# Optimization experiments

Hardware: AMD Instinct MI355X
Metric: run time of the kernel (lower is better)

Reference implementation:

```python
import jax, jax.numpy as jnp
import numpy as np

BSZ, DIM, H, W = 4, 128, 64, 64
D_MODEL = 128
D = 128   # d_expand == d_inner
N = 16    # d_state
R = 8     # dt_rank = ceil(128/16)
K = 4     # scan directions
L = H * W


def _ln_last(x, g, b, eps):
    m = x.mean(-1, keepdims=True)
    v = x.var(-1, keepdims=True)
    return (x - m) * jax.lax.rsqrt(v + eps) * g + b


def _ln_channel(x, g, b, eps):
    # LayerNorm2d: normalize over channel axis of NCHW
    m = x.mean(1, keepdims=True)
    v = x.var(1, keepdims=True)
    return (x - m) * jax.lax.rsqrt(v + eps) * g[None, :, None, None] + b[None, :, None, None]


def _cross_scan(x):
    # x: (B, D, H, W) -> (B, K, D, L); dirs: row-major, col-major, and their reverses
    b, d = x.shape[0], x.shape[1]
    x0 = x.reshape(b, d, L)
    x1 = x.transpose(0, 1, 3, 2).reshape(b, d, L)
    return jnp.stack([x0, x1, x0[..., ::-1], x1[..., ::-1]], axis=1)


def _cross_merge(ys):
    # ys: (B, K, D, L) -> (B, D, L)
    b, _, d, _ = ys.shape
    ys = ys[:, 0:2] + ys[:, 2:4, :, ::-1]
    y1 = ys[:, 1].reshape(b, d, W, H).transpose(0, 1, 3, 2).reshape(b, d, L)
    return ys[:, 0] + y1


def _selective_scan(u, dt, A, Bs, Cs, Dsk):
    # u, dt: (B,K,D,L); A: (K,D,N); Bs, Cs: (B,K,N,L); Dsk: (K,D)
    uT = u.transpose(3, 0, 1, 2)    # (L,B,K,D)
    dtT = dt.transpose(3, 0, 1, 2)
    BT = Bs.transpose(3, 0, 1, 2)   # (L,B,K,N)
    CT = Cs.transpose(3, 0, 1, 2)
    h0 = jnp.zeros((u.shape[0], K, u.shape[2], N), u.dtype)

    def step(h, inp):
        ut, dtt, bt, ct = inp
        dA = jnp.exp(dtt[..., None] * A)                      # (B,K,D,N)
        h = dA * h + (dtt * ut)[..., None] * bt[:, :, None, :]
        y = jnp.sum(h * ct[:, :, None, :], axis=-1)           # (B,K,D)
        return h, y

    _, ysT = jax.lax.scan(step, h0, (uT, dtT, BT, CT))
    ys = ysT.transpose(1, 2, 3, 0)                            # (B,K,D,L)
    return ys + u * Dsk[None, :, :, None]


def _forward(x, in_proj_w, conv_w, conv_b, sa_w, sa_b, x_proj_weight,
             dt_projs_weight, dt_projs_bias, A_logs, Ds,
             out_norm_g, out_norm_b, norm1_g, norm1_b, out_proj_w):
    # in_proj (1x1 conv, no bias) then chunk into x, z
    xz = jnp.einsum('bchw,oc->bohw', x, in_proj_w)
    xi, z = jnp.split(xz, 2, axis=1)
    z1 = jax.nn.gelu(z, approximate=False)
    # depthwise 3x3 conv + bias
    xi = jax.lax.conv_general_dilated(xi, conv_w, (1, 1), 'SAME',
                                      feature_group_count=D,
                                      dimension_numbers=('NCHW', 'OIHW', 'NCHW'))
    xi = xi + conv_b[None, :, None, None]
    xi = jax.nn.gelu(xi, approximate=False)
    # SpatialAttention (CBAM-style): mean+max over channels -> 7x7 conv -> sigmoid gate
    pooled = jnp.concatenate([xi.mean(1, keepdims=True), xi.max(1, keepdims=True)], axis=1)
    attn = jax.lax.conv_general_dilated(pooled, sa_w, (1, 1), 'SAME',
                                        dimension_numbers=('NCHW', 'OIHW', 'NCHW'))
    xi = xi * jax.nn.sigmoid(attn + sa_b[None, :, None, None])
    # cross selective scan
    xs = _cross_scan(xi)                                              # (B,K,D,L)
    x_dbl = jnp.einsum('bkdl,kcd->bkcl', xs, x_proj_weight)           # (B,K,R+2N,L)
    dts, Bs, Cs = x_dbl[:, :, :R], x_dbl[:, :, R:R + N], x_dbl[:, :, R + N:]
    dts = jnp.einsum('bkrl,kdr->bkdl', dts, dt_projs_weight)
    dt = jax.nn.softplus(dts + dt_projs_bias[None, :, :, None])
    A = -jnp.exp(A_logs).reshape(K, D, N)
    ys = _selective_scan(xs, dt, A, Bs, Cs, Ds.reshape(K, D))         # (B,K,D,L)
    y = _cross_merge(ys)                                              # (B,D,L)
    y = y.reshape(-1, D, H, W).transpose(0, 2, 3, 1)                  # (B,H,W,D)
    y = _ln_last(y, out_norm_g, out_norm_b, 1e-5)
    y = y.transpose(0, 3, 1, 2)                                       # (B,D,H,W)
    # z gate, LayerNorm2d, out_proj (1x1 conv)
    y = y * z1
    y = _ln_channel(y, norm1_g, norm1_b, 1e-6)
    return jnp.einsum('bchw,oc->bohw', y, out_proj_w)


def setup_inputs() -> dict:
    key = jax.random.key(0)
    ks = jax.random.split(key, 8)
    s = 0.02
    return {
        'x': jax.random.normal(ks[0], (BSZ, DIM, H, W), jnp.float32),
        'in_proj_w': jax.random.normal(ks[1], (2 * D, DIM), jnp.float32) * s,
        'conv_w': jax.random.normal(ks[2], (D, 1, 3, 3), jnp.float32) * s,
        'conv_b': jnp.zeros((D,), jnp.float32),
        'sa_w': jax.random.normal(ks[3], (1, 2, 7, 7), jnp.float32) * s,
        'sa_b': jnp.zeros((1,), jnp.float32),
        'x_proj_weight': jax.random.normal(ks[4], (K, R + 2 * N, D), jnp.float32) * s,
        'dt_projs_weight': jax.random.normal(ks[5], (K, D, R), jnp.float32) * s,
        'dt_projs_bias': jax.random.normal(ks[6], (K, D), jnp.float32) * s,
        'A_logs': jnp.log(jnp.tile(jnp.arange(1, N + 1, dtype=jnp.float32)[None, :], (K * D, 1))),
        'Ds': jnp.ones((K * D,), jnp.float32),
        'out_norm_g': jnp.ones((D,), jnp.float32),
        'out_norm_b': jnp.zeros((D,), jnp.float32),
        'norm1_g': jnp.ones((D,), jnp.float32),
        'norm1_b': jnp.zeros((D,), jnp.float32),
        'out_proj_w': jax.random.normal(ks[7], (D_MODEL, D), jnp.float32) * s,
    }


def reference(x, in_proj_w, conv_w, conv_b, sa_w, sa_b, x_proj_weight,
              dt_projs_weight, dt_projs_bias, A_logs, Ds,
              out_norm_g, out_norm_b, norm1_g, norm1_b, out_proj_w):
    return _forward(x, in_proj_w, conv_w, conv_b, sa_w, sa_b, x_proj_weight,
                    dt_projs_weight, dt_projs_bias, A_logs, Ds,
                    out_norm_g, out_norm_b, norm1_g, norm1_b, out_proj_w)
```

## Files before the change

### kernel.cpp

```cpp
#include <hip/hip_runtime.h>
#include <math.h>

#define BB   4
#define DD   128
#define LL   4096
#define SEG  128

union F4 { float4 v; float f[4]; };

__device__ __forceinline__ float gelu_f(float x){
  return 0.5f * x * (1.f + erff(x * 0.70710678118654752f));
}
__device__ __forceinline__ float softplus_fast(float x){
  return (x > 20.f) ? x : __logf(1.f + __expf(x));
}

__global__ __launch_bounds__(256) void k_inproj(const float* __restrict__ x,
    const float* __restrict__ W, float* __restrict__ xi, float* __restrict__ z1){
  __shared__ __align__(16) float Xs[128*32];
  int b = blockIdx.z; int half = blockIdx.y; int p0 = blockIdx.x*32;
  int t = threadIdx.x;
  int po = t & 31, row8 = t >> 5;
  for (int j=0;j<16;j++){
    int c = row8 + 8*j;
    Xs[c*32 + po] = x[((size_t)(b*128 + c))*LL + p0 + po];
  }
  __syncthreads();
  int pg = t & 7, og = t >> 3;
  int obase = og*4 + half*128;
  const float4* w0r = (const float4*)&W[(size_t)(obase+0)*128];
  const float4* w1r = (const float4*)&W[(size_t)(obase+1)*128];
  const float4* w2r = (const float4*)&W[(size_t)(obase+2)*128];
  const float4* w3r = (const float4*)&W[(size_t)(obase+3)*128];
  float acc[4][4];
  #pragma unroll
  for (int i=0;i<4;i++){ acc[i][0]=0;acc[i][1]=0;acc[i][2]=0;acc[i][3]=0; }
  for (int c4=0;c4<32;c4++){
    F4 xv[4];
    #pragma unroll
    for (int r=0;r<4;r++) xv[r].v = *(const float4*)&Xs[(c4*4+r)*32 + pg*4];
    F4 wv[4];
    wv[0].v = w0r[c4]; wv[1].v = w1r[c4]; wv[2].v = w2r[c4]; wv[3].v = w3r[c4];
    #pragma unroll
    for (int i=0;i<4;i++)
      #pragma unroll
      for (int q=0;q<4;q++)
        acc[i][q] = fmaf(wv[i].f[3], xv[3].f[q],
                    fmaf(wv[i].f[2], xv[2].f[q],
                    fmaf(wv[i].f[1], xv[1].f[q],
                    fmaf(wv[i].f[0], xv[0].f[q], acc[i][q]))));
  }
  if (half == 0){
    #pragma unroll
    for (int i=0;i<4;i++){
      F4 st; st.f[0]=acc[i][0]; st.f[1]=acc[i][1]; st.f[2]=acc[i][2]; st.f[3]=acc[i][3];
      *(float4*)&xi[((size_t)(b*128+obase+i))*LL + p0 + pg*4] = st.v;
    }
  } else {
    #pragma unroll
    for (int i=0;i<4;i++){
      F4 st; st.f[0]=gelu_f(acc[i][0]); st.f[1]=gelu_f(acc[i][1]);
      st.f[2]=gelu_f(acc[i][2]); st.f[3]=gelu_f(acc[i][3]);
      *(float4*)&z1[((size_t)(b*128+obase-128+i))*LL + p0 + pg*4] = st.v;
    }
  }
}

__global__ __launch_bounds__(256) void k_conv(const float* __restrict__ xi,
    const float* __restrict__ cw, const float* __restrict__ cb, float* __restrict__ xc){
  int idx = blockIdx.x*256 + threadIdx.x;
  int p = idx & 4095; int c = (idx>>12) & 127; int b = idx>>19;
  int y = p>>6, x = p&63;
  const float* src = xi + ((size_t)(b*128+c))*LL;
  float w[9];
  #pragma unroll
  for (int i=0;i<9;i++) w[i] = cw[c*9+i];
  float a = cb[c];
  #pragma unroll
  for (int dy=-1;dy<=1;dy++){
    int yy = y+dy; if (yy<0 || yy>63) continue;
    #pragma unroll
    for (int dx=-1;dx<=1;dx++){
      int xx = x+dx; if (xx<0 || xx>63) continue;
      a = fmaf(w[(dy+1)*3+dx+1], src[yy*64+xx], a);
    }
  }
  xc[((size_t)(b*128+c))*LL + p] = gelu_f(a);
}

__global__ __launch_bounds__(256) void k_pool(const float* __restrict__ xc,
    float* __restrict__ pooled){
  __shared__ float rs[4][64], rm[4][64];
  int b = blockIdx.y; int po = threadIdx.x & 63; int cg = threadIdx.x >> 6;
  int p = blockIdx.x*64 + po;
  const float* src = xc + ((size_t)b*128)*LL + p;
  float s = 0.f, mx = -3.4e38f;
  for (int ci=0;ci<32;ci++){
    float v = src[(size_t)(cg*32+ci)*LL];
    s += v; mx = fmaxf(mx, v);
  }
  rs[cg][po] = s; rm[cg][po] = mx;
  __syncthreads();
  if (cg == 0){
    float ss = rs[0][po]+rs[1][po]+rs[2][po]+rs[3][po];
    float mm = fmaxf(fmaxf(rm[0][po],rm[1][po]),fmaxf(rm[2][po],rm[3][po]));
    pooled[((size_t)(b*2+0))*LL + p] = ss*(1.f/128.f);
    pooled[((size_t)(b*2+1))*LL + p] = mm;
  }
}

__global__ __launch_bounds__(256) void k_attn(const float* __restrict__ pooled,
    const float* __restrict__ saw, const float* __restrict__ sab, float* __restrict__ sig){
  __shared__ float ps[2][10][70];
  int b = blockIdx.y; int p0 = blockIdx.x*256;
  int y0 = p0>>6;
  int t = threadIdx.x;
  for (int e=t; e<1400; e+=256){
    int ic = e/700; int rem = e - ic*700; int r = rem/70; int cc = rem - r*70;
    int gy = y0-3+r, gx = cc-3;
    float v = 0.f;
    if (gy>=0&&gy<64&&gx>=0&&gx<64) v = pooled[((size_t)(b*2+ic))*LL + gy*64+gx];
    ps[ic][r][cc] = v;
  }
  __syncthreads();
  int ry = t>>6, xx = t&63;
  float acc = sab[0];
  #pragma unroll
  for (int ic=0;ic<2;ic++)
    for (int ky=0;ky<7;ky++)
      #pragma unroll
      for (int kx=0;kx<7;kx++)
        acc += saw[ic*49+ky*7+kx] * ps[ic][ry+ky][xx+kx];
  sig[(size_t)b*LL + p0 + t] = 1.f/(1.f+__expf(-acc));
}

__global__ __launch_bounds__(256) void k_gate(const float* __restrict__ xc,
    const float* __restrict__ sig, float* __restrict__ u, float* __restrict__ uT){
  __shared__ float tl[64*65];
  int d = blockIdx.x, b = blockIdx.y;
  const float* src = xc + ((size_t)(b*128+d))*LL;
  const float* sg  = sig + (size_t)b*LL;
  float* du = u  + ((size_t)(b*128+d))*LL;
  float* dT = uT + ((size_t)(b*128+d))*LL;
  int t = threadIdx.x;
  #pragma unroll
  for (int j=0;j<16;j++){
    int idx = t + j*256;
    int r = idx>>6, c = idx&63;
    float v = src[idx]*sg[idx];
    du[idx] = v;
    tl[c*65+r] = v;
  }
  __syncthreads();
  #pragma unroll
  for (int j=0;j<16;j++){
    int idx = t + j*256;
    int r = idx>>6, c = idx&63;
    dT[idx] = tl[r*65+c];
  }
}

__global__ __launch_bounds__(256) void k_gate4(const float* __restrict__ u,
    const float* __restrict__ uT, float* __restrict__ u4){
  __shared__ float T[64*130];
  int tile = blockIdx.x;
  int ori  = blockIdx.y;
  int b    = blockIdx.z;
  const float* src = (ori ? uT : u) + ((size_t)b*128)*LL + tile*64;
  int t = threadIdx.x;
  int po = t&63, dg = t>>6;
  for (int di=0; di<32; di++){
    int d = dg*32+di;
    T[po*130 + d] = src[(size_t)d*LL + po];
  }
  __syncthreads();
  float* dst = u4 + ((size_t)((b*2+ori)*1024) + tile*16)*512;
  #pragma unroll
  for (int j=0;j<8;j++){
    int L = j*1024 + t*4;
    int d = t & 127;
    int pxb = (L >> 9)*4;
    F4 st;
    #pragma unroll
    for (int s=0;s<4;s++) st.f[s] = T[(pxb+s)*130 + d];
    *(float4*)&dst[L] = st.v;
  }
}

__global__ __launch_bounds__(256) void k_xdbl(const float* __restrict__ u,
    const float* __restrict__ uT, const float* __restrict__ xpw,
    float* __restrict__ C8_l, float* __restrict__ Bs_l, float* __restrict__ Cs_l){
  __shared__ __align__(16) float Ws[40*128];
  __shared__ __align__(16) float Xs[64*128];
  __shared__ __align__(16) float Xd[40*128];
  int px0 = blockIdx.x*128;
  int k = blockIdx.y; int b = blockIdx.z; int bk = b*4+k;
  int t = threadIdx.x;
  const float* ub = (k&1) ? uT : u;
  {
    const float4* src = (const float4*)(xpw + (size_t)k*40*128);
    float4* dst = (float4*)Ws;
    #pragma unroll
    for (int j=0;j<5;j++) dst[t + j*256] = src[t + j*256];
  }
  int pg = t&31, rg = t>>5;
  float acc[5][4];
  #pragma unroll
  for (int i=0;i<5;i++){ acc[i][0]=0;acc[i][1]=0;acc[i][2]=0;acc[i][3]=0; }
  for (int h=0;h<2;h++){
    __syncthreads();
    {
      int p4 = t&31, ch = t>>5;
      #pragma unroll
      for (int j=0;j<8;j++){
        int c = ch + j*8;
        F4 v; v.v = *(const float4*)&ub[((size_t)(b*128 + h*64 + c))*LL + px0 + p4*4];
        *(float4*)&Xs[c*128 + p4*4] = v.v;
      }
    }
    __syncthreads();
    const float* wbase = Ws + rg*5*128 + h*64;
    for (int c4=0;c4<16;c4++){
      F4 xv[4];
      #pragma unroll
      for (int r=0;r<4;r++) xv[r].v = *(const float4*)&Xs[(c4*4+r)*128 + pg*4];
      F4 wv[5];
      #pragma unroll
      for (int i=0;i<5;i++) wv[i].v = *(const float4*)(wbase + i*128 + c4*4);
      #pragma unroll
      for (int i=0;i<5;i++)
        #pragma unroll
        for (int q=0;q<4;q++)
          acc[i][q] = fmaf(wv[i].f[3], xv[3].f[q],
                      fmaf(wv[i].f[2], xv[2].f[q],
                      fmaf(wv[i].f[1], xv[1].f[q],
                      fmaf(wv[i].f[0], xv[0].f[q], acc[i][q]))));
    }
  }
  #pragma unroll
  for (int i=0;i<5;i++){
    F4 st; st.f[0]=acc[i][0]; st.f[1]=acc[i][1]; st.f[2]=acc[i][2]; st.f[3]=acc[i][3];
    *(float4*)&Xd[(rg*5+i)*128 + pg*4] = st.v;
  }
  __syncthreads();
  #pragma unroll
  for (int j=0;j<5;j++){
    int idx = t + j*256;
    int row = idx>>5, pq = idx&31;
    F4 v; v.v = *(const float4*)&Xd[row*128 + pq*4];
    float* dst;
    if (row < 8)       dst = C8_l + ((size_t)(bk*8 + row))*LL;
    else if (row < 24) dst = Bs_l + ((size_t)(bk*16 + row-8))*LL;
    else               dst = Cs_l + ((size_t)(bk*16 + row-24))*LL;
    int pp = px0 + pq*4;
    if (k < 2){
      *(float4*)&dst[pp] = v.v;
    } else {
      F4 st; st.f[0]=v.f[3]; st.f[1]=v.f[2]; st.f[2]=v.f[1]; st.f[3]=v.f[0];
      *(float4*)&dst[LL-4-pp] = st.v;
    }
  }
}

__global__ __launch_bounds__(256) void k_dt(const float* __restrict__ C8_l,
    const float* __restrict__ dtw, const float* __restrict__ dtb,
    float* __restrict__ dt4){
  __shared__ __align__(16) F4 c8s[8*16];
  __shared__ float wt[128*9];
  __shared__ float db[128];
  int chunk = blockIdx.x;
  int bk = blockIdx.y; int k = bk&3;
  int t = threadIdx.x;
  int px0 = chunk*64;
  if (t < 128){
    c8s[t].v = *(const float4*)&C8_l[((size_t)(bk*8 + (t>>4)))*LL + px0 + (t&15)*4];
    db[t] = dtb[k*128 + t];
  }
  {
    const float* src = dtw + (size_t)k*128*8;
    #pragma unroll
    for (int j=0;j<4;j++){
      int e = t + j*256;
      wt[(e>>3)*9 + (e&7)] = src[e];
    }
  }
  __syncthreads();
  float* outb = dt4 + ((size_t)(bk*1024 + chunk*16))*512;
  #pragma unroll
  for (int j=0;j<8;j++){
    int idx = j*256 + t;
    int i4l = idx>>7, d = idx&127;
    float dw[8];
    #pragma unroll
    for (int r=0;r<8;r++) dw[r] = wt[d*9+r];
    float bias = db[d];
    float a0=bias, a1=bias, a2=bias, a3=bias;
    #pragma unroll
    for (int r=0;r<8;r++){
      F4 c = c8s[r*16 + i4l];
      a0 = fmaf(dw[r], c.f[0], a0);
      a1 = fmaf(dw[r], c.f[1], a1);
      a2 = fmaf(dw[r], c.f[2], a2);
      a3 = fmaf(dw[r], c.f[3], a3);
    }
    F4 st;
    st.f[0]=softplus_fast(a0); st.f[1]=softplus_fast(a1);
    st.f[2]=softplus_fast(a2); st.f[3]=softplus_fast(a3);
    *(float4*)&outb[(size_t)i4l*512 + d*4] = st.v;
  }
}

__global__ __launch_bounds__(256) void k_scan1(const float* __restrict__ dt4,
    const float* __restrict__ u4,
    const float* __restrict__ Bs_l, const float* __restrict__ A_logs,
    float* __restrict__ Ebuf, float* __restrict__ sdtbuf){
  int t = threadIdx.x;
  int lane = t & 63; int dh = (t>>6)&1; int segl = t>>7;
  int seg = blockIdx.x*2 + segl; int bk = blockIdx.y;
  int b = bk>>2, k = bk&3;
  int d = dh*64 + lane;
  float A2[16];
  {
    const float4* al = (const float4*)&A_logs[((size_t)(k*128+d))*16];
    #pragma unroll
    for (int q=0;q<4;q++){
      F4 v; v.v = al[q];
      #pragma unroll
      for (int e=0;e<4;e++) A2[q*4+e] = -__expf(v.f[e]);
    }
  }
  float h[16];
  #pragma unroll
  for (int n=0;n<16;n++) h[n]=0.f;
  float sumdt = 0.f;
  bool rev = (k >= 2);
  const float* dt4p = dt4 + ((size_t)(bk*1024 + seg*8)*128 + d)*4;
  const float* u4b  = u4 + ((size_t)((b*2+(k&1))*1024))*512 + d*4;
  const float* Bn = Bs_l + ((size_t)bk*16)*LL + seg*32;
  for (int i4=0;i4<8;i4++){
    F4 dtv; dtv.v = *(const float4*)(dt4p + i4*512);
    F4 uv;
    if (!rev) uv.v = *(const float4*)(u4b + (size_t)(seg*8 + i4)*512);
    else { F4 t0; t0.v = *(const float4*)(u4b + (size_t)(1023 - seg*8 - i4)*512);
           uv.f[0]=t0.f[3]; uv.f[1]=t0.f[2]; uv.f[2]=t0.f[1]; uv.f[3]=t0.f[0]; }
    F4 Bq[16];
    #pragma unroll
    for (int n=0;n<16;n++) Bq[n].v = *(const float4*)(Bn + (size_t)n*LL + i4*4);
    #pragma unroll
    for (int s=0;s<4;s++){
      float dt = dtv.f[s], uu = uv.f[s];
      float au = dt*uu;
      #pragma unroll
      for (int n=0;n<16;n++) h[n] = __expf(dt*A2[n])*h[n] + au*Bq[n].f[s];
      sumdt += dt;
    }
  }
  size_t eoff = ((size_t)(bk*128 + d))*SEG + seg;
  float* ep = Ebuf + eoff*16;
  #pragma unroll
  for (int q=0;q<4;q++){
    F4 st; st.f[0]=h[q*4+0]; st.f[1]=h[q*4+1]; st.f[2]=h[q*4+2]; st.f[3]=h[q*4+3];
    *(float4*)(ep + q*4) = st.v;
  }
  sdtbuf[eoff] = sumdt;
}

__global__ __launch_bounds__(128) void k_scan2(const float* __restrict__ Ebuf,
    const float* __restrict__ sdtbuf, const float* __restrict__ A_logs,
    float* __restrict__ hin){
  __shared__ float A0s[16], E0s[16];
  int d = blockIdx.x;
  int bk = blockIdx.y;
  int k = bk&3;
  int t = threadIdx.x; int lane = t & 63; int w = t >> 6;
  size_t base = ((size_t)(bk*128+d))*SEG;
  float A2[16];
  {
    const float4* al = (const float4*)&A_logs[((size_t)(k*128+d))*16];
    #pragma unroll
    for (int q=0;q<4;q++){
      F4 v; v.v = al[q];
      #pragma unroll
      for (int e=0;e<4;e++) A2[q*4+e] = -__expf(v.f[e]);
    }
  }
  float sdt = sdtbuf[base + t];
  float a[16], e[16];
  {
    const float* ep = Ebuf + (base+t)*16;
    #pragma unroll
    for (int q=0;q<4;q++){
      F4 v; v.v = *(const float4*)(ep + q*4);
      #pragma unroll
      for (int ee=0;ee<4;ee++) e[q*4+ee]=v.f[ee];
    }
  }
  #pragma unroll
  for (int n=0;n<16;n++) a[n] = __expf(sdt*A2[n]);
  #pragma unroll
  for (int off=1; off<64; off<<=1){
    #pragma unroll
    for (int n=0;n<16;n++){
      float pa = __shfl_up(a[n], off, 64);
      float pe = __shfl_up(e[n], off, 64);
      if (lane >= off){ e[n] = fmaf(a[n], pe, e[n]); a[n] *= pa; }
    }
  }
  if (t == 63){
    #pragma unroll
    for (int n=0;n<16;n++){ A0s[n] = a[n]; E0s[n] = e[n]; }
  }
  __syncthreads();
  float eex[16], aex[16];
  #pragma unroll
  for (int n=0;n<16;n++){
    float pa = __shfl_up(a[n], 1, 64);
    float pe = __shfl_up(e[n], 1, 64);
    aex[n] = lane ? pa : 1.f;
    eex[n] = lane ? pe : 0.f;
  }
  if (w == 1){
    #pragma unroll
    for (int n=0;n<16;n++) eex[n] = fmaf(aex[n], E0s[n], eex[n]);
  }
  float* hp = hin + (base+t)*16;
  #pragma unroll
  for (int q=0;q<4;q++){
    F4 st;
    #pragma unroll
    for (int ee=0;ee<4;ee++) st.f[ee] = eex[q*4+ee];
    *(float4*)(hp + q*4) = st.v;
  }
}

__global__ __launch_bounds__(256) void k_scan3(const float* __restrict__ dt4,
    const float* __restrict__ u4,
    const float* __restrict__ Bs_l, const float* __restrict__ Cs_l,
    const float* __restrict__ A_logs, const float* __restrict__ Ds,
    const float* __restrict__ hin, float* __restrict__ ys4){
  int t = threadIdx.x;
  int lane = t & 63; int dh = (t>>6)&1; int segl = t>>7;
  int seg = blockIdx.x*2 + segl; int bk = blockIdx.y;
  int b = bk>>2, k = bk&3;
  int d = dh*64 + lane;
  float A2[16];
  {
    const float4* al = (const float4*)&A_logs[((size_t)(k*128+d))*16];
    #pragma unroll
    for (int q=0;q<4;q++){
      F4 v; v.v = al[q];
      #pragma unroll
      for (int e=0;e<4;e++) A2[q*4+e] = -__expf(v.f[e]);
    }
  }
  float h[16];
  {
    const float* hp = hin + (((size_t)(bk*128+d))*SEG + seg)*16;
    #pragma unroll
    for (int q=0;q<4;q++){
      F4 v; v.v = *(const float4*)(hp + q*4);
      #pragma unroll
      for (int e=0;e<4;e++) h[q*4+e]=v.f[e];
    }
  }
  float Dd = Ds[k*128+d];
  bool rev = (k >= 2);
  const float* dt4p = dt4 + ((size_t)(bk*1024 + seg*8)*128 + d)*4;
  const float* u4b  = u4 + ((size_t)((b*2+(k&1))*1024))*512 + d*4;
  const float* Bn = Bs_l + ((size_t)bk*16)*LL + seg*32;
  const float* Cn = Cs_l + ((size_t)bk*16)*LL + seg*32;
  float* yo = ys4 + ((size_t)(bk*1024 + seg*8))*512 + d*4;
  for (int i4=0;i4<8;i4++){
    F4 dtv; dtv.v = *(const float4*)(dt4p + i4*512);
    F4 uv;
    if (!rev) uv.v = *(const float4*)(u4b + (size_t)(seg*8 + i4)*512);
    else { F4 t0; t0.v = *(const float4*)(u4b + (size_t)(1023 - seg*8 - i4)*512);
           uv.f[0]=t0.f[3]; uv.f[1]=t0.f[2]; uv.f[2]=t0.f[1]; uv.f[3]=t0.f[0]; }
    F4 Bq[16], Cq[16];
    #pragma unroll
    for (int n=0;n<16;n++){
      Bq[n].v = *(const float4*)(Bn + (size_t)n*LL + i4*4);
      Cq[n].v = *(const float4*)(Cn + (size_t)n*LL + i4*4);
    }
    F4 yv;
    #pragma unroll
    for (int s=0;s<4;s++){
      float dt = dtv.f[s], uu = uv.f[s];
      float au = dt*uu;
      float y = uu*Dd;
      #pragma unroll
      for (int n=0;n<16;n++){
        h[n] = __expf(dt*A2[n])*h[n] + au*Bq[n].f[s];
        y = fmaf(h[n], Cq[n].f[s], y);
      }
      yv.f[s] = y;
    }
    *(float4*)(yo + (size_t)i4*512) = yv.v;
  }
}

__global__ __launch_bounds__(256) void k_tr13(const float* __restrict__ ys4,
    float* __restrict__ y13){
  __shared__ float T[16*516];
  int xg = blockIdx.x & 15, yb = blockIdx.x >> 4, b = blockIdx.y;
  const float* y1 = ys4 + ((size_t)((b*4+1)*1024))*512;
  const float* y3 = ys4 + ((size_t)((b*4+3)*1024))*512;
  int t = threadIdx.x;
  int d = t & 127;
  #pragma unroll
  for (int rr=0; rr<8; rr++){
    int ri = rr*2 + (t>>7);
    int xi = ri>>2, r = ri&3;
    int i4q = (4*xg+xi)*16 + yb*4 + r;
    F4 v1; v1.v = *(const float4*)(y1 + (size_t)i4q*512 + d*4);
    F4 v3; v3.v = *(const float4*)(y3 + (size_t)(1023-i4q)*512 + d*4);
    #pragma unroll
    for (int s=0;s<4;s++)
      T[(4*r+s)*516 + d*4 + xi] = v1.f[s] + v3.f[3-s];
  }
  __syncthreads();
  float* dst = y13 + ((size_t)b*1024)*512;
  #pragma unroll
  for (int rr=0; rr<8; rr++){
    int j = rr*2 + (t>>7);
    F4 o;
    #pragma unroll
    for (int s=0;s<4;s++) o.f[s] = T[j*516 + d*4 + s];
    int i4p = (yb*16 + j)*16 + xg;
    *(float4*)(dst + (size_t)i4p*512 + d*4) = o.v;
  }
}

__global__ __launch_bounds__(256) void k_final(const float* __restrict__ ys4,
    const float* __restrict__ y13,
    const float* __restrict__ z1, const float* __restrict__ ong, const float* __restrict__ onb,
    const float* __restrict__ n1g, const float* __restrict__ n1b,
    const float* __restrict__ W2, float* __restrict__ out){
  __shared__ __align__(16) float yt[128*36];
  __shared__ float red[8][32], redq[8][32], mv[4][32];
  int b = blockIdx.y; int p0 = blockIdx.x*32;
  int t = threadIdx.x; int po = t&31; int rg = t>>5;
  {
    int row0 = p0>>2;
    const float* y0p = ys4 + ((size_t)((b*4+0)*1024 + row0))*512;
    const float* y2b = ys4 + ((size_t)((b*4+2)*1024))*512;
    const float* ymp = y13 + ((size_t)(b*1024 + row0))*512;
    #pragma unroll
    for (int j=0;j<4;j++){
      int idx = j*256 + t;
      int rloc = idx>>7; int d = idx&127;
      F4 v0; v0.v = *(const float4*)(y0p + (size_t)rloc*512 + d*4);
      F4 vm; vm.v = *(const float4*)(ymp + (size_t)rloc*512 + d*4);
      F4 v2; v2.v = *(const float4*)(y2b + (size_t)(1023-row0-rloc)*512 + d*4);
      #pragma unroll
      for (int s=0;s<4;s++) yt[d*36 + rloc*4 + s] = v0.f[s] + vm.f[s] + v2.f[3-s];
    }
  }
  __syncthreads();
  float s=0.f, sq=0.f;
  for (int j=0;j<16;j++){
    int d = rg + 8*j;
    float v = yt[d*36+po];
    s += v; sq += v*v;
  }
  red[rg][po] = s; redq[rg][po] = sq;
  __syncthreads();
  if (rg==0){
    float sm=0.f, qq=0.f;
    #pragma unroll
    for (int g=0;g<8;g++){ sm += red[g][po]; qq += redq[g][po]; }
    float m = sm*(1.f/128.f);
    float var = qq*(1.f/128.f) - m*m;
    mv[0][po] = m; mv[1][po] = rsqrtf(var + 1e-5f);
  }
  __syncthreads();
  float m1 = mv[0][po], r1 = mv[1][po];
  s=0.f; sq=0.f;
  for (int j=0;j<16;j++){
    int d = rg + 8*j;
    float v = yt[d*36+po];
    float yn = (v-m1)*r1*ong[d] + onb[d];
    float tv = yn * z1[((size_t)(b*128+d))*LL + p0 + po];
    yt[d*36+po] = tv; s += tv; sq += tv*tv;
  }
  red[rg][po] = s; redq[rg][po] = sq;
  __syncthreads();
  if (rg==0){
    float sm=0.f, qq=0.f;
    #pragma unroll
    for (int g=0;g<8;g++){ sm += red[g][po]; qq += redq[g][po]; }
    float m = sm*(1.f/128.f);
    float var = qq*(1.f/128.f) - m*m;
    mv[2][po] = m; mv[3][po] = rsqrtf(var + 1e-6f);
  }
  __syncthreads();
  float m2 = mv[2][po], r2 = mv[3][po];
  for (int j=0;j<16;j++){
    int d = rg + 8*j;
    float tv = yt[d*36+po];
    yt[d*36+po] = (tv-m2)*r2*n1g[d] + n1b[d];
  }
  __syncthreads();
  int pg = t&7, og = t>>3;
  {
    int obase = og*4;
    const float4* w0r = (const float4*)&W2[(size_t)(obase+0)*128];
    const float4* w1r = (const float4*)&W2[(size_t)(obase+1)*128];
    const float4* w2r = (const float4*)&W2[(size_t)(obase+2)*128];
    const float4* w3r = (const float4*)&W2[(size_t)(obase+3)*128];
    float acc[4][4];
    #pragma unroll
    for (int i=0;i<4;i++){ acc[i][0]=0;acc[i][1]=0;acc[i][2]=0;acc[i][3]=0; }
    for (int c4=0;c4<32;c4++){
      F4 xv[4];
      #pragma unroll
      for (int r=0;r<4;r++) xv[r].v = *(const float4*)&yt[(c4*4+r)*36 + pg*4];
      F4 wv[4];
      wv[0].v = w0r[c4]; wv[1].v = w1r[c4]; wv[2].v = w2r[c4]; wv[3].v = w3r[c4];
      #pragma unroll
      for (int i=0;i<4;i++)
        #pragma unroll
        for (int q=0;q<4;q++)
          acc[i][q] = fmaf(wv[i].f[3], xv[3].f[q],
                      fmaf(wv[i].f[2], xv[2].f[q],
                      fmaf(wv[i].f[1], xv[1].f[q],
                      fmaf(wv[i].f[0], xv[0].f[q], acc[i][q]))));
    }
    #pragma unroll
    for (int i=0;i<4;i++){
      F4 st; st.f[0]=acc[i][0]; st.f[1]=acc[i][1]; st.f[2]=acc[i][2]; st.f[3]=acc[i][3];
      *(float4*)&out[((size_t)(b*128+obase+i))*LL + p0 + pg*4] = st.v;
    }
  }
}

extern "C" void kernel_launch(void* const* d_in, const int* in_sizes, int n_in,
                              void* d_out, int out_size, void* d_ws, size_t ws_size,
                              hipStream_t stream) {
  (void)in_sizes; (void)n_in; (void)out_size; (void)ws_size;
  const float* x    = (const float*)d_in[0];
  const float* ipw  = (const float*)d_in[1];
  const float* cw   = (const float*)d_in[2];
  const float* cb   = (const float*)d_in[3];
  const float* saw  = (const float*)d_in[4];
  const float* sab  = (const float*)d_in[5];
  const float* xpw  = (const float*)d_in[6];
  const float* dtw  = (const float*)d_in[7];
  const float* dtb  = (const float*)d_in[8];
  const float* alog = (const float*)d_in[9];
  const float* Dsv  = (const float*)d_in[10];
  const float* ong  = (const float*)d_in[11];
  const float* onb  = (const float*)d_in[12];
  const float* n1g  = (const float*)d_in[13];
  const float* n1b  = (const float*)d_in[14];
  const float* opw  = (const float*)d_in[15];

  float* ws = (float*)d_ws;
  const size_t SZ_BDL = (size_t)BB*128*LL;
  float* xi     = ws;
  float* xc     = xi  + SZ_BDL;
  float* z1     = xc  + SZ_BDL;
  float* pooled = z1  + SZ_BDL;
  float* sg     = pooled + (size_t)BB*2*LL;
  float* u      = sg  + (size_t)BB*LL;
  float* uT     = u   + SZ_BDL;
  float* u4     = uT  + SZ_BDL;
  float* dt4    = u4  + (size_t)BB*2*1024*512;
  float* C8_l   = dt4 + (size_t)BB*4*1024*512;
  float* Bs_l   = C8_l+ (size_t)BB*4*8*LL;
  float* Cs_l   = Bs_l+ (size_t)BB*4*16*LL;
  float* ys4    = Cs_l+ (size_t)BB*4*16*LL;
  float* y13    = ys4 + (size_t)BB*4*1024*512;
  float* sdtb   = y13 + (size_t)BB*1024*512;
  float* Ebuf   = u;
  float* hin    = xi;

  k_inproj<<<dim3(128, 2, BB), 256, 0, stream>>>(x, ipw, xi, z1);
  k_conv  <<<dim3(BB*128*LL/256), 256, 0, stream>>>(xi, cw, cb, xc);
  k_pool  <<<dim3(64, BB), 256, 0, stream>>>(xc, pooled);
  k_attn  <<<dim3(16, BB), 256, 0, stream>>>(pooled, saw, sab, sg);
  k_gate  <<<dim3(DD, BB), 256, 0, stream>>>(xc, sg, u, uT);
  k_gate4 <<<dim3(64, 2, BB), 256, 0, stream>>>(u, uT, u4);
  k_xdbl  <<<dim3(32, 4, BB), 256, 0, stream>>>(u, uT, xpw, C8_l, Bs_l, Cs_l);
  k_dt    <<<dim3(64, BB*4), 256, 0, stream>>>(C8_l, dtw, dtb, dt4);
  k_scan1 <<<dim3(SEG/2, BB*4), 256, 0, stream>>>(dt4, u4, Bs_l, alog, Ebuf, sdtb);
  k_scan2 <<<dim3(128, BB*4), 128, 0, stream>>>(Ebuf, sdtb, alog, hin);
  k_scan3 <<<dim3(SEG/2, BB*4), 256, 0, stream>>>(dt4, u4, Bs_l, Cs_l, alog, Dsv, hin, ys4);
  k_tr13  <<<dim3(64, BB), 256, 0, stream>>>(ys4, y13);
  k_final <<<dim3(128, BB), 256, 0, stream>>>(ys4, y13, z1, ong, onb, n1g, n1b, opw, (float*)d_out);
}
```

Before: 201.6 us.

## Split scan state dimension across lane pairs and use exp2 with prescaled A

The chunked scan kernels now give each (d, segment) pair to two lanes, each holding 8 of the 16 state entries. This halves per-thread registers and doubles the grid, with the output sum combined through a lane shuffle. A is premultiplied by log2(e) so the inner recurrence can use exp2f instead of expf. The change aims to raise occupancy and parallelism in the latency-bound recurrence. In exchange it adds a shuffle per step, makes the two lanes load the same dt and u values redundantly, and leaves half the lanes idle on the y store.

```diff
diff --git a/kernel.cpp b/kernel.cpp
--- a/kernel.cpp
+++ b/kernel.cpp
@@ -14,6 +14,7 @@
 __device__ __forceinline__ float softplus_fast(float x){
   return (x > 20.f) ? x : __logf(1.f + __expf(x));
 }
+#define LOG2E 1.4426950408889634f
 
 __global__ __launch_bounds__(256) void k_inproj(const float* __restrict__ x,
     const float* __restrict__ W, float* __restrict__ xi, float* __restrict__ z1){
@@ -315,54 +316,55 @@
     const float* __restrict__ Bs_l, const float* __restrict__ A_logs,
     float* __restrict__ Ebuf, float* __restrict__ sdtbuf){
   int t = threadIdx.x;
-  int lane = t & 63; int dh = (t>>6)&1; int segl = t>>7;
-  int seg = blockIdx.x*2 + segl; int bk = blockIdx.y;
+  int lane = t & 63; int wv = t >> 6;
+  int seg = blockIdx.x; int bk = blockIdx.y;
   int b = bk>>2, k = bk&3;
-  int d = dh*64 + lane;
-  float A2[16];
-  {
-    const float4* al = (const float4*)&A_logs[((size_t)(k*128+d))*16];
-    #pragma unroll
-    for (int q=0;q<4;q++){
+  int dl = lane >> 1, nh = lane & 1;
+  int d = wv*32 + dl;
+  float A2[8];
+  {
+    const float4* al = (const float4*)&A_logs[((size_t)(k*128+d))*16 + nh*8];
+    #pragma unroll
+    for (int q=0;q<2;q++){
       F4 v; v.v = al[q];
       #pragma unroll
-      for (int e=0;e<4;e++) A2[q*4+e] = -__expf(v.f[e]);
-    }
-  }
-  float h[16];
-  #pragma unroll
-  for (int n=0;n<16;n++) h[n]=0.f;
+      for (int e=0;e<4;e++) A2[q*4+e] = -__expf(v.f[e])*LOG2E;
+    }
+  }
+  float h[8];
+  #pragma unroll
+  for (int n=0;n<8;n++) h[n]=0.f;
   float sumdt = 0.f;
   bool rev = (k >= 2);
   const float* dt4p = dt4 + ((size_t)(bk*1024 + seg*8)*128 + d)*4;
   const float* u4b  = u4 + ((size_t)((b*2+(k&1))*1024))*512 + d*4;
-  const float* Bn = Bs_l + ((size_t)bk*16)*LL + seg*32;
+  const float* Bn = Bs_l + ((size_t)(bk*16 + nh*8))*LL + seg*32;
   for (int i4=0;i4<8;i4++){
     F4 dtv; dtv.v = *(const float4*)(dt4p + i4*512);
     F4 uv;
     if (!rev) uv.v = *(const float4*)(u4b + (size_t)(seg*8 + i4)*512);
     else { F4 t0; t0.v = *(const float4*)(u4b + (size_t)(1023 - seg*8 - i4)*512);
            uv.f[0]=t0.f[3]; uv.f[1]=t0.f[2]; uv.f[2]=t0.f[1]; uv.f[3]=t0.f[0]; }
-    F4 Bq[16];
-    #pragma unroll
-    for (int n=0;n<16;n++) Bq[n].v = *(const float4*)(Bn + (size_t)n*LL + i4*4);
+    F4 Bq[8];
+    #pragma unroll
+    for (int n=0;n<8;n++) Bq[n].v = *(const float4*)(Bn + (size_t)n*LL + i4*4);
     #pragma unroll
     for (int s=0;s<4;s++){
       float dt = dtv.f[s], uu = uv.f[s];
       float au = dt*uu;
       #pragma unroll
-      for (int n=0;n<16;n++) h[n] = __expf(dt*A2[n])*h[n] + au*Bq[n].f[s];
+      for (int n=0;n<8;n++) h[n] = exp2f(dt*A2[n])*h[n] + au*Bq[n].f[s];
       sumdt += dt;
     }
   }
   size_t eoff = ((size_t)(bk*128 + d))*SEG + seg;
-  float* ep = Ebuf + eoff*16;
-  #pragma unroll
-  for (int q=0;q<4;q++){
+  float* ep = Ebuf + eoff*16 + nh*8;
+  #pragma unroll
+  for (int q=0;q<2;q++){
     F4 st; st.f[0]=h[q*4+0]; st.f[1]=h[q*4+1]; st.f[2]=h[q*4+2]; st.f[3]=h[q*4+3];
     *(float4*)(ep + q*4) = st.v;
   }
-  sdtbuf[eoff] = sumdt;
+  if (nh == 0) sdtbuf[eoff] = sumdt;
 }
 
 __global__ __launch_bounds__(128) void k_scan2(const float* __restrict__ Ebuf,
@@ -381,7 +383,7 @@
     for (int q=0;q<4;q++){
       F4 v; v.v = al[q];
       #pragma unroll
-      for (int e=0;e<4;e++) A2[q*4+e] = -__expf(v.f[e]);
+      for (int e=0;e<4;e++) A2[q*4+e] = -__expf(v.f[e])*LOG2E;
     }
   }
   float sdt = sdtbuf[base + t];
@@ -396,7 +398,7 @@
     }
   }
   #pragma unroll
-  for (int n=0;n<16;n++) a[n] = __expf(sdt*A2[n]);
+  for (int n=0;n<16;n++) a[n] = exp2f(sdt*A2[n]);
   #pragma unroll
   for (int off=1; off<64; off<<=1){
     #pragma unroll
@@ -439,36 +441,37 @@
     const float* __restrict__ A_logs, const float* __restrict__ Ds,
     const float* __restrict__ hin, float* __restrict__ ys4){
   int t = threadIdx.x;
-  int lane = t & 63; int dh = (t>>6)&1; int segl = t>>7;
-  int seg = blockIdx.x*2 + segl; int bk = blockIdx.y;
+  int lane = t & 63; int wv = t >> 6;
+  int seg = blockIdx.x; int bk = blockIdx.y;
   int b = bk>>2, k = bk&3;
-  int d = dh*64 + lane;
-  float A2[16];
-  {
-    const float4* al = (const float4*)&A_logs[((size_t)(k*128+d))*16];
-    #pragma unroll
-    for (int q=0;q<4;q++){
+  int dl = lane >> 1, nh = lane & 1;
+  int d = wv*32 + dl;
+  float A2[8];
+  {
+    const float4* al = (const float4*)&A_logs[((size_t)(k*128+d))*16 + nh*8];
+    #pragma unroll
+    for (int q=0;q<2;q++){
       F4 v; v.v = al[q];
       #pragma unroll
-      for (int e=0;e<4;e++) A2[q*4+e] = -__expf(v.f[e]);
-    }
-  }
-  float h[16];
-  {
-    const float* hp = hin + (((size_t)(bk*128+d))*SEG + seg)*16;
-    #pragma unroll
-    for (int q=0;q<4;q++){
+      for (int e=0;e<4;e++) A2[q*4+e] = -__expf(v.f[e])*LOG2E;
+    }
+  }
+  float h[8];
+  {
+    const float* hp = hin + (((size_t)(bk*128+d))*SEG + seg)*16 + nh*8;
+    #pragma unroll
+    for (int q=0;q<2;q++){
       F4 v; v.v = *(const float4*)(hp + q*4);
       #pragma unroll
       for (int e=0;e<4;e++) h[q*4+e]=v.f[e];
     }
   }
-  float Dd = Ds[k*128+d];
+  float Dd = (nh==0) ? Ds[k*128+d] : 0.f;
   bool rev = (k >= 2);
   const float* dt4p = dt4 + ((size_t)(bk*1024 + seg*8)*128 + d)*4;
   const float* u4b  = u4 + ((size_t)((b*2+(k&1))*1024))*512 + d*4;
-  const float* Bn = Bs_l + ((size_t)bk*16)*LL + seg*32;
-  const float* Cn = Cs_l + ((size_t)bk*16)*LL + seg*32;
+  const float* Bn = Bs_l + ((size_t)(bk*16 + nh*8))*LL + seg*32;
+  const float* Cn = Cs_l + ((size_t)(bk*16 + nh*8))*LL + seg*32;
   float* yo = ys4 + ((size_t)(bk*1024 + seg*8))*512 + d*4;
   for (int i4=0;i4<8;i4++){
     F4 dtv; dtv.v = *(const float4*)(dt4p + i4*512);
@@ -476,9 +479,9 @@
     if (!rev) uv.v = *(const float4*)(u4b + (size_t)(seg*8 + i4)*512);
     else { F4 t0; t0.v = *(const float4*)(u4b + (size_t)(1023 - seg*8 - i4)*512);
            uv.f[0]=t0.f[3]; uv.f[1]=t0.f[2]; uv.f[2]=t0.f[1]; uv.f[3]=t0.f[0]; }
-    F4 Bq[16], Cq[16];
-    #pragma unroll
-    for (int n=0;n<16;n++){
+    F4 Bq[8], Cq[8];
+    #pragma unroll
+    for (int n=0;n<8;n++){
       Bq[n].v = *(const float4*)(Bn + (size_t)n*LL + i4*4);
       Cq[n].v = *(const float4*)(Cn + (size_t)n*LL + i4*4);
     }
@@ -489,13 +492,14 @@
       float au = dt*uu;
       float y = uu*Dd;
       #pragma unroll
-      for (int n=0;n<16;n++){
-        h[n] = __expf(dt*A2[n])*h[n] + au*Bq[n].f[s];
+      for (int n=0;n<8;n++){
+        h[n] = exp2f(dt*A2[n])*h[n] + au*Bq[n].f[s];
         y = fmaf(h[n], Cq[n].f[s], y);
       }
+      y += __shfl_xor(y, 1, 64);
       yv.f[s] = y;
     }
-    *(float4*)(yo + (size_t)i4*512) = yv.v;
+    if (nh == 0) *(float4*)(yo + (size_t)i4*512) = yv.v;
   }
 }
 
@@ -683,9 +687,9 @@
   k_gate4 <<<dim3(64, 2, BB), 256, 0, stream>>>(u, uT, u4);
   k_xdbl  <<<dim3(32, 4, BB), 256, 0, stream>>>(u, uT, xpw, C8_l, Bs_l, Cs_l);
   k_dt    <<<dim3(64, BB*4), 256, 0, stream>>>(C8_l, dtw, dtb, dt4);
-  k_scan1 <<<dim3(SEG/2, BB*4), 256, 0, stream>>>(dt4, u4, Bs_l, alog, Ebuf, sdtb);
+  k_scan1 <<<dim3(SEG, BB*4), 256, 0, stream>>>(dt4, u4, Bs_l, alog, Ebuf, sdtb);
   k_scan2 <<<dim3(128, BB*4), 128, 0, stream>>>(Ebuf, sdtb, alog, hin);
-  k_scan3 <<<dim3(SEG/2, BB*4), 256, 0, stream>>>(dt4, u4, Bs_l, Cs_l, alog, Dsv, hin, ys4);
+  k_scan3 <<<dim3(SEG, BB*4), 256, 0, stream>>>(dt4, u4, Bs_l, Cs_l, alog, Dsv, hin, ys4);
   k_tr13  <<<dim3(64, BB), 256, 0, stream>>>(ys4, y13);
   k_final <<<dim3(128, BB), 256, 0, stream>>>(ys4, y13, z1, ong, onb, n1g, n1b, opw, (float*)d_out);
 }
```

After: 284.0 us. 1.41x slower.

## Double scan segment count, split state buffers, use exp2 in scan

Applied to the files above, without the earlier changes.

Doubles the number of chunked-scan segments from 128 to 256, so each thread scans 16 timesteps instead of 32 and twice as many blocks run the serial chunk scans. The segment-prefix kernel now combines four wavefronts through shared memory, and the chunk-state buffers are split into two workspace regions so the larger buffer fits. It also folds log2(e) into A so the inner loop can call exp2f. In exchange, more chunk states are written and read and the cross-segment combine step does more work.

```diff
diff --git a/kernel.cpp b/kernel.cpp
--- a/kernel.cpp
+++ b/kernel.cpp
@@ -4,7 +4,7 @@
 #define BB   4
 #define DD   128
 #define LL   4096
-#define SEG  128
+#define SEG  256
 
 union F4 { float4 v; float f[4]; };
 
@@ -14,6 +14,7 @@
 __device__ __forceinline__ float softplus_fast(float x){
   return (x > 20.f) ? x : __logf(1.f + __expf(x));
 }
+#define LOG2E 1.4426950408889634f
 
 __global__ __launch_bounds__(256) void k_inproj(const float* __restrict__ x,
     const float* __restrict__ W, float* __restrict__ xi, float* __restrict__ z1){
@@ -313,7 +314,7 @@
 __global__ __launch_bounds__(256) void k_scan1(const float* __restrict__ dt4,
     const float* __restrict__ u4,
     const float* __restrict__ Bs_l, const float* __restrict__ A_logs,
-    float* __restrict__ Ebuf, float* __restrict__ sdtbuf){
+    float* __restrict__ Elo, float* __restrict__ Ehi, float* __restrict__ sdtbuf){
   int t = threadIdx.x;
   int lane = t & 63; int dh = (t>>6)&1; int segl = t>>7;
   int seg = blockIdx.x*2 + segl; int bk = blockIdx.y;
@@ -326,7 +327,7 @@
     for (int q=0;q<4;q++){
       F4 v; v.v = al[q];
       #pragma unroll
-      for (int e=0;e<4;e++) A2[q*4+e] = -__expf(v.f[e]);
+      for (int e=0;e<4;e++) A2[q*4+e] = -__expf(v.f[e])*LOG2E;
     }
   }
   float h[16];
@@ -334,14 +335,14 @@
   for (int n=0;n<16;n++) h[n]=0.f;
   float sumdt = 0.f;
   bool rev = (k >= 2);
-  const float* dt4p = dt4 + ((size_t)(bk*1024 + seg*8)*128 + d)*4;
+  const float* dt4p = dt4 + ((size_t)(bk*1024 + seg*4)*128 + d)*4;
   const float* u4b  = u4 + ((size_t)((b*2+(k&1))*1024))*512 + d*4;
-  const float* Bn = Bs_l + ((size_t)bk*16)*LL + seg*32;
-  for (int i4=0;i4<8;i4++){
+  const float* Bn = Bs_l + ((size_t)bk*16)*LL + seg*16;
+  for (int i4=0;i4<4;i4++){
     F4 dtv; dtv.v = *(const float4*)(dt4p + i4*512);
     F4 uv;
-    if (!rev) uv.v = *(const float4*)(u4b + (size_t)(seg*8 + i4)*512);
-    else { F4 t0; t0.v = *(const float4*)(u4b + (size_t)(1023 - seg*8 - i4)*512);
+    if (!rev) uv.v = *(const float4*)(u4b + (size_t)(seg*4 + i4)*512);
+    else { F4 t0; t0.v = *(const float4*)(u4b + (size_t)(1023 - seg*4 - i4)*512);
            uv.f[0]=t0.f[3]; uv.f[1]=t0.f[2]; uv.f[2]=t0.f[1]; uv.f[3]=t0.f[0]; }
     F4 Bq[16];
     #pragma unroll
@@ -351,29 +352,31 @@
       float dt = dtv.f[s], uu = uv.f[s];
       float au = dt*uu;
       #pragma unroll
-      for (int n=0;n<16;n++) h[n] = __expf(dt*A2[n])*h[n] + au*Bq[n].f[s];
+      for (int n=0;n<16;n++) h[n] = exp2f(dt*A2[n])*h[n] + au*Bq[n].f[s];
       sumdt += dt;
     }
   }
-  size_t eoff = ((size_t)(bk*128 + d))*SEG + seg;
-  float* ep = Ebuf + eoff*16;
+  float* Eb = (bk < 8) ? Elo : Ehi;
+  size_t eloc = ((size_t)((bk&7)*128 + d))*SEG + seg;
+  float* ep = Eb + eloc*16;
   #pragma unroll
   for (int q=0;q<4;q++){
     F4 st; st.f[0]=h[q*4+0]; st.f[1]=h[q*4+1]; st.f[2]=h[q*4+2]; st.f[3]=h[q*4+3];
     *(float4*)(ep + q*4) = st.v;
   }
-  sdtbuf[eoff] = sumdt;
-}
-
-__global__ __launch_bounds__(128) void k_scan2(const float* __restrict__ Ebuf,
-    const float* __restrict__ sdtbuf, const float* __restrict__ A_logs,
-    float* __restrict__ hin){
-  __shared__ float A0s[16], E0s[16];
+  sdtbuf[((size_t)(bk*128 + d))*SEG + seg] = sumdt;
+}
+
+__global__ __launch_bounds__(256) void k_scan2(float* __restrict__ Elo,
+    float* __restrict__ Ehi,
+    const float* __restrict__ sdtbuf, const float* __restrict__ A_logs){
+  __shared__ float As[4][16], Es[4][16];
   int d = blockIdx.x;
   int bk = blockIdx.y;
   int k = bk&3;
   int t = threadIdx.x; int lane = t & 63; int w = t >> 6;
-  size_t base = ((size_t)(bk*128+d))*SEG;
+  float* Eb = (bk < 8) ? Elo : Ehi;
+  size_t base = ((size_t)((bk&7)*128+d))*SEG;
   float A2[16];
   {
     const float4* al = (const float4*)&A_logs[((size_t)(k*128+d))*16];
@@ -381,13 +384,13 @@
     for (int q=0;q<4;q++){
       F4 v; v.v = al[q];
       #pragma unroll
-      for (int e=0;e<4;e++) A2[q*4+e] = -__expf(v.f[e]);
-    }
-  }
-  float sdt = sdtbuf[base + t];
+      for (int e=0;e<4;e++) A2[q*4+e] = -__expf(v.f[e])*LOG2E;
+    }
+  }
+  float sdt = sdtbuf[((size_t)(bk*128+d))*SEG + t];
   float a[16], e[16];
   {
-    const float* ep = Ebuf + (base+t)*16;
+    const float* ep = Eb + (base+t)*16;
     #pragma unroll
     for (int q=0;q<4;q++){
       F4 v; v.v = *(const float4*)(ep + q*4);
@@ -396,7 +399,7 @@
     }
   }
   #pragma unroll
-  for (int n=0;n<16;n++) a[n] = __expf(sdt*A2[n]);
+  for (int n=0;n<16;n++) a[n] = exp2f(sdt*A2[n]);
   #pragma unroll
   for (int off=1; off<64; off<<=1){
     #pragma unroll
@@ -406,29 +409,33 @@
       if (lane >= off){ e[n] = fmaf(a[n], pe, e[n]); a[n] *= pa; }
     }
   }
-  if (t == 63){
-    #pragma unroll
-    for (int n=0;n<16;n++){ A0s[n] = a[n]; E0s[n] = e[n]; }
-  }
-  __syncthreads();
-  float eex[16], aex[16];
-  #pragma unroll
-  for (int n=0;n<16;n++){
-    float pa = __shfl_up(a[n], 1, 64);
-    float pe = __shfl_up(e[n], 1, 64);
-    aex[n] = lane ? pa : 1.f;
-    eex[n] = lane ? pe : 0.f;
-  }
-  if (w == 1){
-    #pragma unroll
-    for (int n=0;n<16;n++) eex[n] = fmaf(aex[n], E0s[n], eex[n]);
-  }
-  float* hp = hin + (base+t)*16;
+  if (lane == 63){
+    #pragma unroll
+    for (int n=0;n<16;n++){ As[w][n] = a[n]; Es[w][n] = e[n]; }
+  }
+  __syncthreads();
+  float Ec[16];
+  #pragma unroll
+  for (int n=0;n<16;n++) Ec[n] = 0.f;
+  for (int wp=0; wp<3; wp++){
+    if (wp < w){
+      #pragma unroll
+      for (int n=0;n<16;n++) Ec[n] = fmaf(As[wp][n], Ec[n], Es[wp][n]);
+    }
+  }
+  float* hp = Eb + (base+t)*16;
   #pragma unroll
   for (int q=0;q<4;q++){
     F4 st;
     #pragma unroll
-    for (int ee=0;ee<4;ee++) st.f[ee] = eex[q*4+ee];
+    for (int ee=0;ee<4;ee++){
+      int n = q*4+ee;
+      float pa = __shfl_up(a[n], 1, 64);
+      float pe = __shfl_up(e[n], 1, 64);
+      float aex = lane ? pa : 1.f;
+      float eex = lane ? pe : 0.f;
+      st.f[ee] = fmaf(aex, Ec[n], eex);
+    }
     *(float4*)(hp + q*4) = st.v;
   }
 }
@@ -437,7 +444,8 @@
     const float* __restrict__ u4,
     const float* __restrict__ Bs_l, const float* __restrict__ Cs_l,
     const float* __restrict__ A_logs, const float* __restrict__ Ds,
-    const float* __restrict__ hin, float* __restrict__ ys4){
+    const float* __restrict__ Elo, const float* __restrict__ Ehi,
+    float* __restrict__ ys4){
   int t = threadIdx.x;
   int lane = t & 63; int dh = (t>>6)&1; int segl = t>>7;
   int seg = blockIdx.x*2 + segl; int bk = blockIdx.y;
@@ -450,12 +458,13 @@
     for (int q=0;q<4;q++){
       F4 v; v.v = al[q];
       #pragma unroll
-      for (int e=0;e<4;e++) A2[q*4+e] = -__expf(v.f[e]);
+      for (int e=0;e<4;e++) A2[q*4+e] = -__expf(v.f[e])*LOG2E;
     }
   }
   float h[16];
   {
-    const float* hp = hin + (((size_t)(bk*128+d))*SEG + seg)*16;
+    const float* Eb = (bk < 8) ? Elo : Ehi;
+    const float* hp = Eb + (((size_t)((bk&7)*128+d))*SEG + seg)*16;
     #pragma unroll
     for (int q=0;q<4;q++){
       F4 v; v.v = *(const float4*)(hp + q*4);
@@ -465,16 +474,16 @@
   }
   float Dd = Ds[k*128+d];
   bool rev = (k >= 2);
-  const float* dt4p = dt4 + ((size_t)(bk*1024 + seg*8)*128 + d)*4;
+  const float* dt4p = dt4 + ((size_t)(bk*1024 + seg*4)*128 + d)*4;
   const float* u4b  = u4 + ((size_t)((b*2+(k&1))*1024))*512 + d*4;
-  const float* Bn = Bs_l + ((size_t)bk*16)*LL + seg*32;
-  const float* Cn = Cs_l + ((size_t)bk*16)*LL + seg*32;
-  float* yo = ys4 + ((size_t)(bk*1024 + seg*8))*512 + d*4;
-  for (int i4=0;i4<8;i4++){
+  const float* Bn = Bs_l + ((size_t)bk*16)*LL + seg*16;
+  const float* Cn = Cs_l + ((size_t)bk*16)*LL + seg*16;
+  float* yo = ys4 + ((size_t)(bk*1024 + seg*4))*512 + d*4;
+  for (int i4=0;i4<4;i4++){
     F4 dtv; dtv.v = *(const float4*)(dt4p + i4*512);
     F4 uv;
-    if (!rev) uv.v = *(const float4*)(u4b + (size_t)(seg*8 + i4)*512);
-    else { F4 t0; t0.v = *(const float4*)(u4b + (size_t)(1023 - seg*8 - i4)*512);
+    if (!rev) uv.v = *(const float4*)(u4b + (size_t)(seg*4 + i4)*512);
+    else { F4 t0; t0.v = *(const float4*)(u4b + (size_t)(1023 - seg*4 - i4)*512);
            uv.f[0]=t0.f[3]; uv.f[1]=t0.f[2]; uv.f[2]=t0.f[1]; uv.f[3]=t0.f[0]; }
     F4 Bq[16], Cq[16];
     #pragma unroll
@@ -490,7 +499,7 @@
       float y = uu*Dd;
       #pragma unroll
       for (int n=0;n<16;n++){
-        h[n] = __expf(dt*A2[n])*h[n] + au*Bq[n].f[s];
+        h[n] = exp2f(dt*A2[n])*h[n] + au*Bq[n].f[s];
         y = fmaf(h[n], Cq[n].f[s], y);
       }
       yv.f[s] = y;
@@ -672,8 +681,8 @@
   float* ys4    = Cs_l+ (size_t)BB*4*16*LL;
   float* y13    = ys4 + (size_t)BB*4*1024*512;
   float* sdtb   = y13 + (size_t)BB*1024*512;
-  float* Ebuf   = u;
-  float* hin    = xi;
+  float* Elo    = u;
+  float* Ehi    = xi;
 
   k_inproj<<<dim3(128, 2, BB), 256, 0, stream>>>(x, ipw, xi, z1);
   k_conv  <<<dim3(BB*128*LL/256), 256, 0, stream>>>(xi, cw, cb, xc);
@@ -683,9 +692,9 @@
   k_gate4 <<<dim3(64, 2, BB), 256, 0, stream>>>(u, uT, u4);
   k_xdbl  <<<dim3(32, 4, BB), 256, 0, stream>>>(u, uT, xpw, C8_l, Bs_l, Cs_l);
   k_dt    <<<dim3(64, BB*4), 256, 0, stream>>>(C8_l, dtw, dtb, dt4);
-  k_scan1 <<<dim3(SEG/2, BB*4), 256, 0, stream>>>(dt4, u4, Bs_l, alog, Ebuf, sdtb);
-  k_scan2 <<<dim3(128, BB*4), 128, 0, stream>>>(Ebuf, sdtb, alog, hin);
-  k_scan3 <<<dim3(SEG/2, BB*4), 256, 0, stream>>>(dt4, u4, Bs_l, Cs_l, alog, Dsv, hin, ys4);
+  k_scan1 <<<dim3(SEG/2, BB*4), 256, 0, stream>>>(dt4, u4, Bs_l, alog, Elo, Ehi, sdtb);
+  k_scan2 <<<dim3(128, BB*4), 256, 0, stream>>>(Elo, Ehi, sdtb, alog);
+  k_scan3 <<<dim3(SEG/2, BB*4), 256, 0, stream>>>(dt4, u4, Bs_l, Cs_l, alog, Dsv, Elo, Ehi, ys4);
   k_tr13  <<<dim3(64, BB), 256, 0, stream>>>(ys4, y13);
   k_final <<<dim3(128, BB), 256, 0, stream>>>(ys4, y13, z1, ong, onb, n1g, n1b, opw, (float*)d_out);
 }
```

Result: slower. 286.5 us (+42.2%).
